# Kernel tuning notes

Hardware: AMD Instinct MI355X
Metric: run time of the kernel (lower is better)

The kernel has to match this reference:

```python
import jax, jax.numpy as jnp
import numpy as np

GAMMA = 1.0
ALPHA = 0.5
EPS = 1e-8


def setup_inputs() -> dict:
    key = jax.random.key(0)
    k1, k2 = jax.random.split(key)
    x = jax.random.normal(k1, (2048, 32), dtype=jnp.float32)
    y = jax.random.normal(k2, (2048, 32), dtype=jnp.float32)
    return {"x": x, "y": y}


def _normalize(a):
    # torch: mean/std over batch dim, std is unbiased (ddof=1)
    mu = jnp.mean(a, axis=0, keepdims=True)
    sd = jnp.std(a, axis=0, ddof=1, keepdims=True)
    return (a - mu) / (sd + EPS)


def reference(x, y):
    # Classical RBF kernel on normalized inputs
    xn = _normalize(x)
    yn = _normalize(y)
    d = xn[:, None, :] - yn[None, :, :]            # [N, M, D]
    classical = jnp.exp(-GAMMA * jnp.sum(d * d, axis=-1))  # [N, M]

    # Quantum kernel, analytic closed form:
    # RY(t)|0> = [cos(t/2), sin(t/2)]; product state overlap ->
    # |<psi_x|psi_y>|^2 = prod_i cos^2((x_i - y_i)/2)
    qd = (x[:, None, :] - y[None, :, :]) * 0.5     # [N, M, D]
    quantum = jnp.prod(jnp.square(jnp.cos(qd)), axis=-1)    # [N, M]

    return (1.0 - ALPHA) * classical + ALPHA * quantum
```

## Files before the change

### kernel.cpp

```cpp
#include <hip/hip_runtime.h>
#include <math.h>

#define NROWS 2048
#define DDIM 32
#define SBLK 16
#define SROWS (NROWS / SBLK)

typedef __attribute__((ext_vector_type(8))) short short8;
typedef __attribute__((ext_vector_type(4))) float f32x4;

__global__ __launch_bounds__(256) void HybridKernel_stats_partial(
    const float* __restrict__ x, const float* __restrict__ y,
    float* __restrict__ part) {
  const int b = blockIdx.x;
  const int a = b >> 4;
  const int blk = b & (SBLK - 1);
  const float* in = a ? y : x;
  const int t = threadIdx.x;
  const int col = t & 31;
  const int rg = t >> 5;
  float s = 0.f, s2 = 0.f;
  const int r0 = blk * SROWS + rg;
#pragma unroll
  for (int i = 0; i < SROWS / 8; ++i) {
    float v = in[(r0 + i * 8) * DDIM + col];
    s += v;
    s2 = fmaf(v, v, s2);
  }
  __shared__ float ss[8][32];
  __shared__ float sq[8][32];
  ss[rg][col] = s;
  sq[rg][col] = s2;
  __syncthreads();
  if (t < 32) {
    float S = 0.f, Q = 0.f;
#pragma unroll
    for (int g = 0; g < 8; ++g) {
      S += ss[g][t];
      Q += sq[g][t];
    }
    part[b * 64 + t] = S;
    part[b * 64 + 32 + t] = Q;
  }
}

__device__ __forceinline__ unsigned packbf(float a, float b) {
  return (__float_as_uint(a) >> 16) | (__float_as_uint(b) & 0xffff0000u);
}

__global__ __launch_bounds__(512, 2) void HybridKernel_main(
    const float* __restrict__ x, const float* __restrict__ y,
    const float* __restrict__ part, float* __restrict__ out) {
  __shared__ float4 sCS[2][16 * 128];
  __shared__ uint4 sXB[2][2][128 * 5];
  __shared__ float sNrm[2][128];
  __shared__ float sMu[2][32];
  __shared__ float sInv[2][32];

  const int t = threadIdx.x;
  const int i0 = blockIdx.y * 128;
  const int j0 = blockIdx.x * 128;

  float4 gx[2], gy[2];
#pragma unroll
  for (int rep = 0; rep < 2; ++rep) {
    const int u = t + 512 * rep;
    const int row = u >> 3;
    const int q = u & 7;
    gx[rep] = *reinterpret_cast<const float4*>(&x[(i0 + row) * DDIM + q * 4]);
    gy[rep] = *reinterpret_cast<const float4*>(&y[(j0 + row) * DDIM + q * 4]);
  }

  if (t < 64) {
    const int a = t >> 5;
    const int c = t & 31;
    float S = 0.f, Q = 0.f;
#pragma unroll
    for (int bb = 0; bb < SBLK; ++bb) {
      S += part[(a * SBLK + bb) * 64 + c];
      Q += part[(a * SBLK + bb) * 64 + 32 + c];
    }
    const float n = (float)NROWS;
    const float mean = S / n;
    const float var = fmaxf((Q - S * mean) / (n - 1.f), 0.f);
    sMu[a][c] = mean;
    sInv[a][c] = 1.f / (sqrtf(var) + 1e-8f);
  }
  __syncthreads();

#pragma unroll
  for (int rep = 0; rep < 2; ++rep) {
    const int u = t + 512 * rep;
    const int row = u >> 3;
    const int q = u & 7;
#pragma unroll
    for (int side = 0; side < 2; ++side) {
      const float4 g = side ? gy[rep] : gx[rep];
      const float sc = side ? 1.0f : 0.5f;
      const float gv[4] = {g.x, g.y, g.z, g.w};
      float xn[4], hc[4], hs[4];
      float nrm = 0.f;
#pragma unroll
      for (int k = 0; k < 4; ++k) {
        const int d = q * 4 + k;
        xn[k] = (gv[k] - sMu[side][d]) * sInv[side][d];
        nrm = fmaf(xn[k], xn[k], nrm);
        float sn, cs;
        __sincosf(gv[k], &sn, &cs);
        hc[k] = sc * cs;
        hs[k] = sc * sn;
      }
      const int dp0 = 2 * q, dp1 = 2 * q + 1;
      sCS[side][dp0 * 128 + (row ^ (dp0 & 7))] =
          make_float4(hc[0], hs[0], hc[1], hs[1]);
      sCS[side][dp1 * 128 + (row ^ (dp1 & 7))] =
          make_float4(hc[2], hs[2], hc[3], hs[3]);
      float hif[4], lof[4];
#pragma unroll
      for (int k = 0; k < 4; ++k) {
        hif[k] = __uint_as_float(__float_as_uint(xn[k]) & 0xffff0000u);
        lof[k] = xn[k] - hif[k];
      }
      char* bh = (char*)&sXB[side][0][0] + row * 80 + q * 8;
      char* bl = (char*)&sXB[side][1][0] + row * 80 + q * 8;
      *reinterpret_cast<uint2*>(bh) =
          make_uint2(packbf(hif[0], hif[1]), packbf(hif[2], hif[3]));
      *reinterpret_cast<uint2*>(bl) =
          make_uint2(packbf(lof[0], lof[1]), packbf(lof[2], lof[3]));
      nrm += __shfl_xor(nrm, 1);
      nrm += __shfl_xor(nrm, 2);
      nrm += __shfl_xor(nrm, 4);
      if ((t & 7) == 0) sNrm[side][row] = nrm;
    }
  }
  __syncthreads();

  const int w = t >> 6;
  const int l = t & 63;
  const int l4 = l >> 4;
  const int ln = l & 15;
  const int R0 = (w >> 1) * 32;
  const int C0 = (w & 1) * 64;

  short8 Ah[2], Al[2], Bh[4], Bl[4];
  {
    const char* bxh = (const char*)&sXB[0][0][0];
    const char* bxl = (const char*)&sXB[0][1][0];
    const char* byh = (const char*)&sXB[1][0][0];
    const char* byl = (const char*)&sXB[1][1][0];
#pragma unroll
    for (int tr = 0; tr < 2; ++tr) {
      const int off = (R0 + 16 * tr + ln) * 80 + l4 * 16;
      Ah[tr] = *reinterpret_cast<const short8*>(bxh + off);
      Al[tr] = *reinterpret_cast<const short8*>(bxl + off);
    }
#pragma unroll
    for (int tc = 0; tc < 4; ++tc) {
      const int off = (C0 + 16 * tc + ln) * 80 + l4 * 16;
      Bh[tc] = *reinterpret_cast<const short8*>(byh + off);
      Bl[tc] = *reinterpret_cast<const short8*>(byl + off);
    }
  }
  f32x4 dotacc[2][4];
#pragma unroll
  for (int tr = 0; tr < 2; ++tr)
#pragma unroll
    for (int tc = 0; tc < 4; ++tc) {
      f32x4 a = {0.f, 0.f, 0.f, 0.f};
      a = __builtin_amdgcn_mfma_f32_16x16x32_bf16(Ah[tr], Bl[tc], a, 0, 0, 0);
      a = __builtin_amdgcn_mfma_f32_16x16x32_bf16(Al[tr], Bh[tc], a, 0, 0, 0);
      a = __builtin_amdgcn_mfma_f32_16x16x32_bf16(Ah[tr], Bh[tc], a, 0, 0, 0);
      dotacc[tr][tc] = a;
    }

  int r_idx[8], c_idx[4];
#pragma unroll
  for (int ri = 0; ri < 8; ++ri)
    r_idx[ri] = R0 + 16 * (ri >> 2) + 4 * l4 + (ri & 3);
#pragma unroll
  for (int tc = 0; tc < 4; ++tc) c_idx[tc] = C0 + 16 * tc + ln;

  float cl[8][4];
#pragma unroll
  for (int tr = 0; tr < 2; ++tr) {
#pragma unroll
    for (int mm = 0; mm < 4; ++mm) {
      const float nx = sNrm[0][r_idx[tr * 4 + mm]];
#pragma unroll
      for (int tc = 0; tc < 4; ++tc) {
        const float ny = sNrm[1][c_idx[tc]];
        cl[tr * 4 + mm][tc] =
            __expf(2.f * dotacc[tr][tc][mm] - nx - ny);
      }
    }
  }

  const float4* sCS0 = &sCS[0][0];
  const float4* sCS1 = &sCS[1][0];
  float qp[8][4];
#pragma unroll
  for (int ri = 0; ri < 8; ++ri)
#pragma unroll
    for (int tc = 0; tc < 4; ++tc) qp[ri][tc] = 1.f;

#pragma unroll
  for (int dp = 0; dp < 16; ++dp) {
    const int sw = dp & 7;
    float4 FX[8], FY[4];
#pragma unroll
    for (int ri = 0; ri < 8; ++ri)
      FX[ri] = sCS0[dp * 128 + (r_idx[ri] ^ sw)];
#pragma unroll
    for (int tc = 0; tc < 4; ++tc)
      FY[tc] = sCS1[dp * 128 + (c_idx[tc] ^ sw)];
#pragma unroll
    for (int ri = 0; ri < 8; ++ri)
#pragma unroll
      for (int tc = 0; tc < 4; ++tc) {
        const float t0 =
            fmaf(FX[ri].x, FY[tc].x, fmaf(FX[ri].y, FY[tc].y, 0.5f));
        const float t1 =
            fmaf(FX[ri].z, FY[tc].z, fmaf(FX[ri].w, FY[tc].w, 0.5f));
        qp[ri][tc] *= t0 * t1;
      }
  }

#pragma unroll
  for (int ri = 0; ri < 8; ++ri) {
    float* o = out + (size_t)(i0 + r_idx[ri]) * NROWS + j0;
#pragma unroll
    for (int tc = 0; tc < 4; ++tc) {
      o[c_idx[tc]] = 0.5f * (cl[ri][tc] + qp[ri][tc]);
    }
  }
}

extern "C" void kernel_launch(void* const* d_in, const int* in_sizes, int n_in,
                              void* d_out, int out_size, void* d_ws,
                              size_t ws_size, hipStream_t stream) {
  const float* x = (const float*)d_in[0];
  const float* y = (const float*)d_in[1];
  float* part = (float*)d_ws;
  float* out = (float*)d_out;

  HybridKernel_stats_partial<<<2 * SBLK, 256, 0, stream>>>(x, y, part);
  dim3 grid(NROWS / 128, NROWS / 128);
  HybridKernel_main<<<grid, 512, 0, stream>>>(x, y, part, out);
}
```

Baseline: 24.55 us.

## Fuse column statistics into main kernel, recomputing per block

Drops the separate stats kernel launch. Each 128x128 tile block now reads all of x and y (2048x32 each) to compute column means and stds itself, reducing through shared memory. This saves a launch and the dependency between the two kernels, but adds 512 KB of redundant reads per block (served mostly from L2) and extra shared memory, which may lower occupancy.

```diff
diff --git a/kernel.cpp b/kernel.cpp
--- a/kernel.cpp
+++ b/kernel.cpp
@@ -3,56 +3,21 @@
 
 #define NROWS 2048
 #define DDIM 32
-#define SBLK 16
-#define SROWS (NROWS / SBLK)
 
 typedef __attribute__((ext_vector_type(8))) short short8;
 typedef __attribute__((ext_vector_type(4))) float f32x4;
-
-__global__ __launch_bounds__(256) void HybridKernel_stats_partial(
-    const float* __restrict__ x, const float* __restrict__ y,
-    float* __restrict__ part) {
-  const int b = blockIdx.x;
-  const int a = b >> 4;
-  const int blk = b & (SBLK - 1);
-  const float* in = a ? y : x;
-  const int t = threadIdx.x;
-  const int col = t & 31;
-  const int rg = t >> 5;
-  float s = 0.f, s2 = 0.f;
-  const int r0 = blk * SROWS + rg;
-#pragma unroll
-  for (int i = 0; i < SROWS / 8; ++i) {
-    float v = in[(r0 + i * 8) * DDIM + col];
-    s += v;
-    s2 = fmaf(v, v, s2);
-  }
-  __shared__ float ss[8][32];
-  __shared__ float sq[8][32];
-  ss[rg][col] = s;
-  sq[rg][col] = s2;
-  __syncthreads();
-  if (t < 32) {
-    float S = 0.f, Q = 0.f;
-#pragma unroll
-    for (int g = 0; g < 8; ++g) {
-      S += ss[g][t];
-      Q += sq[g][t];
-    }
-    part[b * 64 + t] = S;
-    part[b * 64 + 32 + t] = Q;
-  }
-}
 
 __device__ __forceinline__ unsigned packbf(float a, float b) {
   return (__float_as_uint(a) >> 16) | (__float_as_uint(b) & 0xffff0000u);
 }
 
-__global__ __launch_bounds__(512, 2) void HybridKernel_main(
+__global__ __launch_bounds__(512, 2) void HybridKernel_fused(
     const float* __restrict__ x, const float* __restrict__ y,
-    const float* __restrict__ part, float* __restrict__ out) {
+    float* __restrict__ out) {
   __shared__ float4 sCS[2][16 * 128];
   __shared__ uint4 sXB[2][2][128 * 5];
+  __shared__ float4 sRed[2][64][8];
+  __shared__ float4 sRedQ[2][64][8];
   __shared__ float sNrm[2][128];
   __shared__ float sMu[2][32];
   __shared__ float sInv[2][32];
@@ -71,23 +36,6 @@
     gy[rep] = *reinterpret_cast<const float4*>(&y[(j0 + row) * DDIM + q * 4]);
   }
 
-  if (t < 64) {
-    const int a = t >> 5;
-    const int c = t & 31;
-    float S = 0.f, Q = 0.f;
-#pragma unroll
-    for (int bb = 0; bb < SBLK; ++bb) {
-      S += part[(a * SBLK + bb) * 64 + c];
-      Q += part[(a * SBLK + bb) * 64 + 32 + c];
-    }
-    const float n = (float)NROWS;
-    const float mean = S / n;
-    const float var = fmaxf((Q - S * mean) / (n - 1.f), 0.f);
-    sMu[a][c] = mean;
-    sInv[a][c] = 1.f / (sqrtf(var) + 1e-8f);
-  }
-  __syncthreads();
-
 #pragma unroll
   for (int rep = 0; rep < 2; ++rep) {
     const int u = t + 512 * rep;
@@ -98,13 +46,9 @@
       const float4 g = side ? gy[rep] : gx[rep];
       const float sc = side ? 1.0f : 0.5f;
       const float gv[4] = {g.x, g.y, g.z, g.w};
-      float xn[4], hc[4], hs[4];
-      float nrm = 0.f;
+      float hc[4], hs[4];
 #pragma unroll
       for (int k = 0; k < 4; ++k) {
-        const int d = q * 4 + k;
-        xn[k] = (gv[k] - sMu[side][d]) * sInv[side][d];
-        nrm = fmaf(xn[k], xn[k], nrm);
         float sn, cs;
         __sincosf(gv[k], &sn, &cs);
         hc[k] = sc * cs;
@@ -115,6 +59,92 @@
           make_float4(hc[0], hs[0], hc[1], hs[1]);
       sCS[side][dp1 * 128 + (row ^ (dp1 & 7))] =
           make_float4(hc[2], hs[2], hc[3], hs[3]);
+    }
+  }
+
+  {
+    const int cq = t & 7;
+    const int rg = t >> 3;
+    const float4* px = reinterpret_cast<const float4*>(x) + rg * 8 + cq;
+    const float4* py = reinterpret_cast<const float4*>(y) + rg * 8 + cq;
+    float4 sx = {0.f, 0.f, 0.f, 0.f}, qx = {0.f, 0.f, 0.f, 0.f};
+    float4 sy = {0.f, 0.f, 0.f, 0.f}, qy = {0.f, 0.f, 0.f, 0.f};
+#pragma unroll 4
+    for (int i = 0; i < NROWS / 64; ++i) {
+      const float4 vx = px[(size_t)i * 64 * 8];
+      const float4 vy = py[(size_t)i * 64 * 8];
+      sx.x += vx.x; qx.x = fmaf(vx.x, vx.x, qx.x);
+      sx.y += vx.y; qx.y = fmaf(vx.y, vx.y, qx.y);
+      sx.z += vx.z; qx.z = fmaf(vx.z, vx.z, qx.z);
+      sx.w += vx.w; qx.w = fmaf(vx.w, vx.w, qx.w);
+      sy.x += vy.x; qy.x = fmaf(vy.x, vy.x, qy.x);
+      sy.y += vy.y; qy.y = fmaf(vy.y, vy.y, qy.y);
+      sy.z += vy.z; qy.z = fmaf(vy.z, vy.z, qy.z);
+      sy.w += vy.w; qy.w = fmaf(vy.w, vy.w, qy.w);
+    }
+    sRed[0][rg][cq] = sx;
+    sRedQ[0][rg][cq] = qx;
+    sRed[1][rg][cq] = sy;
+    sRedQ[1][rg][cq] = qy;
+  }
+  __syncthreads();
+  if (t < 128) {
+    const int a = t >> 6;
+    const int g8 = (t >> 3) & 7;
+    const int cq = t & 7;
+    float4 S = {0.f, 0.f, 0.f, 0.f}, Q = {0.f, 0.f, 0.f, 0.f};
+#pragma unroll
+    for (int k = 0; k < 8; ++k) {
+      const float4 a1 = sRed[a][g8 * 8 + k][cq];
+      const float4 b1 = sRedQ[a][g8 * 8 + k][cq];
+      S.x += a1.x; S.y += a1.y; S.z += a1.z; S.w += a1.w;
+      Q.x += b1.x; Q.y += b1.y; Q.z += b1.z; Q.w += b1.w;
+    }
+    sRed[a][g8][cq] = S;
+    sRedQ[a][g8][cq] = Q;
+  }
+  __syncthreads();
+  if (t < 16) {
+    const int a = t >> 3;
+    const int cq = t & 7;
+    float4 S = {0.f, 0.f, 0.f, 0.f}, Q = {0.f, 0.f, 0.f, 0.f};
+#pragma unroll
+    for (int k = 0; k < 8; ++k) {
+      const float4 a1 = sRed[a][k][cq];
+      const float4 b1 = sRedQ[a][k][cq];
+      S.x += a1.x; S.y += a1.y; S.z += a1.z; S.w += a1.w;
+      Q.x += b1.x; Q.y += b1.y; Q.z += b1.z; Q.w += b1.w;
+    }
+    const float Sa[4] = {S.x, S.y, S.z, S.w};
+    const float Qa[4] = {Q.x, Q.y, Q.z, Q.w};
+    const float n = (float)NROWS;
+#pragma unroll
+    for (int k = 0; k < 4; ++k) {
+      const float mean = Sa[k] / n;
+      const float var = fmaxf((Qa[k] - Sa[k] * mean) / (n - 1.f), 0.f);
+      sMu[a][cq * 4 + k] = mean;
+      sInv[a][cq * 4 + k] = 1.f / (sqrtf(var) + 1e-8f);
+    }
+  }
+  __syncthreads();
+
+#pragma unroll
+  for (int rep = 0; rep < 2; ++rep) {
+    const int u = t + 512 * rep;
+    const int row = u >> 3;
+    const int q = u & 7;
+#pragma unroll
+    for (int side = 0; side < 2; ++side) {
+      const float4 g = side ? gy[rep] : gx[rep];
+      const float gv[4] = {g.x, g.y, g.z, g.w};
+      float xn[4];
+      float nrm = 0.f;
+#pragma unroll
+      for (int k = 0; k < 4; ++k) {
+        const int d = q * 4 + k;
+        xn[k] = (gv[k] - sMu[side][d]) * sInv[side][d];
+        nrm = fmaf(xn[k], xn[k], nrm);
+      }
       float hif[4], lof[4];
 #pragma unroll
       for (int k = 0; k < 4; ++k) {
@@ -189,8 +219,7 @@
 #pragma unroll
       for (int tc = 0; tc < 4; ++tc) {
         const float ny = sNrm[1][c_idx[tc]];
-        cl[tr * 4 + mm][tc] =
-            __expf(2.f * dotacc[tr][tc][mm] - nx - ny);
+        cl[tr * 4 + mm][tc] = __expf(2.f * dotacc[tr][tc][mm] - nx - ny);
       }
     }
   }
@@ -208,11 +237,9 @@
     const int sw = dp & 7;
     float4 FX[8], FY[4];
 #pragma unroll
-    for (int ri = 0; ri < 8; ++ri)
-      FX[ri] = sCS0[dp * 128 + (r_idx[ri] ^ sw)];
-#pragma unroll
-    for (int tc = 0; tc < 4; ++tc)
-      FY[tc] = sCS1[dp * 128 + (c_idx[tc] ^ sw)];
+    for (int ri = 0; ri < 8; ++ri) FX[ri] = sCS0[dp * 128 + (r_idx[ri] ^ sw)];
+#pragma unroll
+    for (int tc = 0; tc < 4; ++tc) FY[tc] = sCS1[dp * 128 + (c_idx[tc] ^ sw)];
 #pragma unroll
     for (int ri = 0; ri < 8; ++ri)
 #pragma unroll
@@ -240,10 +267,8 @@
                               size_t ws_size, hipStream_t stream) {
   const float* x = (const float*)d_in[0];
   const float* y = (const float*)d_in[1];
-  float* part = (float*)d_ws;
   float* out = (float*)d_out;
 
-  HybridKernel_stats_partial<<<2 * SBLK, 256, 0, stream>>>(x, y, part);
   dim3 grid(NROWS / 128, NROWS / 128);
-  HybridKernel_main<<<grid, 512, 0, stream>>>(x, y, part, out);
+  HybridKernel_fused<<<grid, 512, 0, stream>>>(x, y, out);
 }
```

Measured after the change: 24.26 us. Within noise of the previous version (-1.2%).
